# Performance work log

Measured on AMD Instinct MI355X. Metric: run time of the kernel, lower is better.

The kernel has to match this reference:

```python
import jax, jax.numpy as jnp
import numpy as np
from jax.scipy.special import logsumexp

B, T, F = 32, 256, 32   # batch, line width (time), line height (features)
HID = 128
VOCAB = 100             # blank index = VOCAB
LBL = 32                # label length
NEG = -1e30


def _mdlstm(x, Wx, Wh1, Wh2, b):
    # x: [B, H, W, C] -> 2D LSTM: outer scan over width, inner scan over height
    Bb, H, W, C = x.shape
    hid = Wh1.shape[0]

    def col_step(carry, x_col):
        c_left, h_left = carry  # [H, B, hid] states from previous column

        def row_step(rc, inp):
            c_up, h_up = rc          # [B, hid] from previous row
            x_ij, c_l, h_l = inp     # [B, C], [B, hid], [B, hid]
            z = x_ij @ Wx + h_l @ Wh1 + h_up @ Wh2 + b  # [B, 5*hid]
            i_, g_, f1, f2, o_ = jnp.split(z, 5, axis=-1)
            c = jax.nn.sigmoid(f1) * c_l + jax.nn.sigmoid(f2) * c_up + jax.nn.sigmoid(i_) * jnp.tanh(g_)
            h = jax.nn.sigmoid(o_) * jnp.tanh(c)
            return (c, h), (c, h)

        z0 = jnp.zeros((Bb, hid), x.dtype)
        _, (c_col, h_col) = jax.lax.scan(row_step, (z0, z0), (x_col, c_left, h_left))
        return (c_col, h_col), h_col

    x_t = jnp.transpose(x, (2, 1, 0, 3))  # [W, H, B, C]
    zc = jnp.zeros((H, Bb, hid), x.dtype)
    _, hs = jax.lax.scan(col_step, (zc, zc), x_t)  # [W, H, B, hid]
    return jnp.transpose(hs, (2, 1, 0, 3))  # [B, H, W, hid]


def _ctc_loss(logp, labels, blank):
    # logp: [B, T, V] log-softmax; labels: [B, L] int in [0, blank)
    Bb, Tt, V = logp.shape
    Ll = labels.shape[1]
    S = 2 * Ll + 1
    ext = jnp.full((Bb, S), blank, dtype=labels.dtype).at[:, 1::2].set(labels)  # blank-interleaved
    lp_ext = jnp.take_along_axis(logp, jnp.broadcast_to(ext[:, None, :], (Bb, Tt, S)), axis=2)  # [B,T,S]
    prev2 = jnp.concatenate([jnp.full((Bb, 2), blank, dtype=ext.dtype), ext[:, :-2]], axis=1)
    skip = (ext != blank) & (ext != prev2)
    skip = skip.at[:, :2].set(False)
    alpha0 = jnp.full((Bb, S), NEG, logp.dtype).at[:, 0].set(lp_ext[:, 0, 0]).at[:, 1].set(lp_ext[:, 0, 1])

    def step(alpha, lp_t):
        a1 = jnp.concatenate([jnp.full((Bb, 1), NEG, alpha.dtype), alpha[:, :-1]], axis=1)
        a2 = jnp.concatenate([jnp.full((Bb, 2), NEG, alpha.dtype), alpha[:, :-2]], axis=1)
        a2 = jnp.where(skip, a2, NEG)
        new = logsumexp(jnp.stack([alpha, a1, a2], axis=0), axis=0) + lp_t
        return new, None

    alphaT, _ = jax.lax.scan(step, alpha0, jnp.transpose(lp_ext, (1, 0, 2))[1:])
    ll = logsumexp(jnp.stack([alphaT[:, -1], alphaT[:, -2]], axis=0), axis=0)
    return -ll  # [B]


def setup_inputs() -> dict:
    key = jax.random.key(0)
    ks = jax.random.split(key, 8)
    s = 0.08
    return {
        "X": jax.random.normal(ks[0], (B, T, F), jnp.float32),
        "y": jax.random.randint(ks[1], (B, LBL), 0, VOCAB),
        "Wx": jax.random.normal(ks[2], (1, 5 * HID), jnp.float32) * s,
        "Wh1": jax.random.normal(ks[3], (HID, 5 * HID), jnp.float32) * s,
        "Wh2": jax.random.normal(ks[4], (HID, 5 * HID), jnp.float32) * s,
        "b": jax.random.normal(ks[5], (5 * HID,), jnp.float32) * 0.01,
        "W_fc": jax.random.normal(ks[6], (HID, VOCAB + 1), jnp.float32) * s,
        "b_fc": jax.random.normal(ks[7], (VOCAB + 1,), jnp.float32) * 0.01,
    }


def reference(X, y, Wx, Wh1, Wh2, b, W_fc, b_fc):
    x = jnp.transpose(X, (0, 2, 1))[..., None]        # [B, F, T, 1] (image)
    h = _mdlstm(x, Wx, Wh1, Wh2, b)                    # [B, F, T, HID]
    feat = jnp.sum(h, axis=1)                          # collapse over height -> [B, T, HID]
    logits = feat @ W_fc + b_fc                        # [B, T, VOCAB+1]
    logp = jax.nn.log_softmax(logits, axis=-1)
    return _ctc_loss(logp, y, VOCAB)                   # per-example CTC loss [B]
```

## Files before the change

kernel.cpp:

```cpp
#include <hip/hip_runtime.h>

#define NEGF (-1e30f)

typedef __attribute__((ext_vector_type(8))) short short8;
typedef __attribute__((ext_vector_type(4))) float float4v;

template <bool V> struct BC { static constexpr bool value = V; };

__device__ __forceinline__ short f2bf(float f) {
  union { float f; unsigned u; } v; v.f = f;
  unsigned r = v.u + 0x7fffu + ((v.u >> 16) & 1u);
  return (short)(r >> 16);
}
__device__ __forceinline__ float fastrcp(float x) { return __builtin_amdgcn_rcpf(x); }
__device__ __forceinline__ float sigf(float x) { return fastrcp(1.0f + __expf(-x)); }
__device__ __forceinline__ float tanhfast(float x) { return 1.0f - 2.0f * fastrcp(__expf(2.0f * x) + 1.0f); }

__global__ void prep_w_kernel(const float* __restrict__ Wh1, const float* __restrict__ Wh2,
                              short* __restrict__ wsW) {
  int t = blockIdx.x * 256 + threadIdx.x;
  int lane = t & 63;
  int frag = t >> 6;
  int nt = frag >> 3, kk = frag & 7;
  int n  = nt * 16 + (lane & 15);
  int kb = kk * 32 + (lane >> 4) * 8;
  short8 v;
#pragma unroll
  for (int j = 0; j < 8; ++j) {
    int k = kb + j;
    float w = (k < 128) ? Wh1[k * 640 + n] : Wh2[(k - 128) * 640 + n];
    v[j] = f2bf(w);
  }
  ((short8*)wsW)[frag * 64 + lane] = v;
}

__global__ __launch_bounds__(512)
void mdlstm_kernel(const float* __restrict__ X, const short* __restrict__ wsW,
                   const float* __restrict__ Wx, const float* __restrict__ bias,
                   float* __restrict__ feat) {
  __shared__ __align__(16) short h_buf[2][32][136];
  __shared__ __align__(16) short wlds[128 * 512];

  const int b    = blockIdx.x;
  const int tid  = threadIdx.x;
  const int lane = tid & 63;
  const int g    = tid >> 6;
  const int col  = lane & 15;
  const int quad = lane >> 4;
  const int jj   = g * 16 + col;

  for (int i = tid; i < 2 * 32 * 136 / 2; i += 512) ((int*)h_buf)[i] = 0;
  {
    const uint4* src = (const uint4*)(wsW + 192 * 512);
    uint4* dst = (uint4*)wlds;
    for (int i = tid; i < 8192; i += 512) dst[i] = src[i];
  }
  {
    float4 z4 = {0.f, 0.f, 0.f, 0.f};
    float4* f4 = (float4*)(feat + b * 32768);
    for (int i = tid; i < 8192; i += 512) f4[i] = z4;
  }

  float wx[5], bg[5];
#pragma unroll
  for (int q = 0; q < 5; ++q) {
    wx[q] = Wx[q * 128 + jj];
    bg[q] = bias[q * 128 + jj];
  }
  float cp[2][4];
#pragma unroll
  for (int mt = 0; mt < 2; ++mt)
#pragma unroll
    for (int r = 0; r < 4; ++r) cp[mt][r] = 0.0f;

  const float* Xg = X + b * 8192;
  float* fb = feat + b * 32768;
  const short8* W8 = (const short8*)wsW;
  const int col48 = col + 48;
  __syncthreads();

  auto step = [&](int d, auto c0, auto c1, auto cv) {
    constexpr bool DO0 = decltype(c0)::value;
    constexpr bool DO1 = decltype(c1)::value;
    constexpr bool ALLV = decltype(cv)::value;
    const int rbuf = (d + 1) & 1, wbuf = d & 1;

    float4v acc[5][2];
#pragma unroll
    for (int q = 0; q < 5; ++q) {
      if (DO0) acc[q][0] = (float4v){bg[q], bg[q], bg[q], bg[q]};
      if (DO1) acc[q][1] = (float4v){bg[q], bg[q], bg[q], bg[q]};
    }
    const short8 z8 = (short8){0, 0, 0, 0, 0, 0, 0, 0};
#pragma unroll
    for (int kk = 0; kk < 8; ++kk) {
      const int up = (kk >= 4) ? 1 : 0;
      const int cc = (kk & 3) * 32 + quad * 8;
      short8 a0, a1;
      if (DO0) {
        int row = col - up;
        a0 = (row >= 0) ? *(const short8*)&h_buf[rbuf][row][cc] : z8;
      }
      if (DO1) {
        int row = 16 + col - up;
        a1 = *(const short8*)&h_buf[rbuf][row][cc];
      }
#pragma unroll
      for (int q = 0; q < 5; ++q) {
        short8 bf;
        if (q < 3) bf = W8[((q * 8 + g) * 8 + kk) * 64 + lane];
        else       bf = *(const short8*)&wlds[(((q - 3) * 8 + g) * 8 + kk) * 512 + lane * 8];
        if (DO0) acc[q][0] = __builtin_amdgcn_mfma_f32_16x16x32_bf16(a0, bf, acc[q][0], 0, 0, 0);
        if (DO1) acc[q][1] = __builtin_amdgcn_mfma_f32_16x16x32_bf16(a1, bf, acc[q][1], 0, 0, 0);
      }
    }

    float t0 = __shfl_up(cp[0][3], 16);
    float t1 = __shfl_up(cp[1][3], 16);
    float tx = __shfl(cp[0][3], col48);
    float cuA[4] = {quad ? t0 : 0.0f, cp[0][0], cp[0][1], cp[0][2]};
    float cuB[4] = {quad ? t1 : tx,   cp[1][0], cp[1][1], cp[1][2]};

    float fo[2][4], xm[2][4];
#pragma unroll
    for (int mt = 0; mt < 2; ++mt) {
      if ((mt == 0 && !DO0) || (mt == 1 && !DO1)) continue;
      const int m0 = mt * 16 + quad * 4;
#pragma unroll
      for (int r = 0; r < 4; ++r) {
        int w = d - (m0 + r);
        if (ALLV || (w >= 0 && w < 256)) {
          fo[mt][r] = fb[w * 128 + jj];
          xm[mt][r] = Xg[w * 32 + (m0 + r)];
        }
      }
    }
#pragma unroll
    for (int mt = 0; mt < 2; ++mt) {
      if ((mt == 0 && !DO0) || (mt == 1 && !DO1)) continue;
      const int m0 = mt * 16 + quad * 4;
#pragma unroll
      for (int r = 0; r < 4; ++r) {
        const int m = m0 + r;
        const int w = d - m;
        if (ALLV || (w >= 0 && w < 256)) {
          float c_up = mt ? cuB[r] : cuA[r];
          float c_l  = cp[mt][r];
          float x    = xm[mt][r];
          float zi = fmaf(x, wx[0], acc[0][mt][r]);
          float zg = fmaf(x, wx[1], acc[1][mt][r]);
          float z1 = fmaf(x, wx[2], acc[2][mt][r]);
          float z2 = fmaf(x, wx[3], acc[3][mt][r]);
          float zo = fmaf(x, wx[4], acc[4][mt][r]);
          float c = sigf(z1) * c_l + sigf(z2) * c_up + sigf(zi) * tanhfast(zg);
          float h = sigf(zo) * tanhfast(c);
          cp[mt][r] = c;
          h_buf[wbuf][m][jj] = f2bf(h);
          fb[w * 128 + jj] = fo[mt][r] + h;
        }
      }
    }
  };

  BC<true> T; BC<false> F;
  for (int d = 0;   d < 16;  ++d) { step(d, T, F, F); __syncthreads(); }
  for (int d = 16;  d < 31;  ++d) { step(d, T, T, F); __syncthreads(); }
  for (int d = 31;  d < 256; ++d) { step(d, T, T, T); __syncthreads(); }
  for (int d = 256; d < 271; ++d) { step(d, T, T, F); __syncthreads(); }
  for (int d = 271; d < 287; ++d) { step(d, F, T, F); __syncthreads(); }
}

__global__ __launch_bounds__(256)
void logits_kernel(const float* __restrict__ feat, const float* __restrict__ Wfc,
                   const float* __restrict__ bfc, float* __restrict__ logp) {
  __shared__ float sW[128 * 101];
  __shared__ float sF[8][128];
  __shared__ float sL[8][104];
  __shared__ float sLse[8];
  const int tid = threadIdx.x;
  const int b  = blockIdx.x >> 5;
  const int t0 = (blockIdx.x & 31) * 8;

  for (int i = tid; i < 128 * 101; i += 256) sW[i] = Wfc[i];
  for (int i = tid; i < 8 * 128; i += 256)
    sF[i >> 7][i & 127] = feat[(b * 256 + t0 + (i >> 7)) * 128 + (i & 127)];
  __syncthreads();
  for (int idx = tid; idx < 8 * 101; idx += 256) {
    int tr = idx / 101, v = idx - tr * 101;
    float s = bfc[v];
#pragma unroll 4
    for (int k = 0; k < 128; ++k) s += sF[tr][k] * sW[k * 101 + v];
    sL[tr][v] = s;
  }
  __syncthreads();
  if (tid < 8) {
    float m = NEGF;
    for (int v = 0; v < 101; ++v) m = fmaxf(m, sL[tid][v]);
    float su = 0.0f;
    for (int v = 0; v < 101; ++v) su += __expf(sL[tid][v] - m);
    sLse[tid] = m + __logf(su);
  }
  __syncthreads();
  for (int idx = tid; idx < 8 * 101; idx += 256) {
    int tr = idx / 101, v = idx - tr * 101;
    logp[(b * 256 + t0 + tr) * 101 + v] = sL[tr][v] - sLse[tr];
  }
}

__global__ __launch_bounds__(64)
void ctc_kernel(const float* __restrict__ logp, const int* __restrict__ y,
                float* __restrict__ out) {
  const int b = blockIdx.x;
  const int l = threadIdx.x;
  const float* lpb = logp + b * 256 * 101;
  const int* yb = y + b * 32;
  int lab = (l & 1) ? yb[l >> 1] : 100;
  bool skip = (l & 1) && (l >= 3) && (yb[l >> 1] != yb[(l >> 1) - 1]);

  float a   = (l == 0) ? lpb[100] : ((l == 1) ? lpb[lab] : NEGF);
  float a64 = NEGF;
  float pl[4], pb[4];
#pragma unroll
  for (int tt = 0; tt < 4; ++tt) {
    pl[tt] = lpb[(1 + tt) * 101 + lab];
    pb[tt] = lpb[(1 + tt) * 101 + 100];
  }
#pragma unroll 4
  for (int t = 1; t < 256; ++t) {
    const int s = (t - 1) & 3;
    float lpl = pl[s], lpbk = pb[s];
    if (t + 4 < 256) {
      pl[s] = lpb[(t + 4) * 101 + lab];
      pb[s] = lpb[(t + 4) * 101 + 100];
    }
    float am1 = __shfl_up(a, 1); if (l == 0) am1 = NEGF;
    float am2 = __shfl_up(a, 2); if (l < 2 || !skip) am2 = NEGF;
    float m3 = fmaxf(a, fmaxf(am1, am2));
    float na = m3 + __logf(__expf(a - m3) + __expf(am1 - m3) + __expf(am2 - m3)) + lpl;
    float m2 = fmaxf(a64, a);
    float na64 = m2 + __logf(__expf(a64 - m2) + __expf(a - m2)) + lpbk;
    a = na;
    a64 = na64;
  }
  float A63 = __shfl(a, 63);
  float A64 = __shfl(a64, 63);
  if (l == 0) {
    float m = fmaxf(A63, A64);
    out[b] = -(m + __logf(__expf(A63 - m) + __expf(A64 - m)));
  }
}

extern "C" void kernel_launch(void* const* d_in, const int* in_sizes, int n_in,
                              void* d_out, int out_size, void* d_ws, size_t ws_size,
                              hipStream_t stream) {
  const float* X   = (const float*)d_in[0];
  const int*   y   = (const int*)d_in[1];
  const float* Wx  = (const float*)d_in[2];
  const float* Wh1 = (const float*)d_in[3];
  const float* Wh2 = (const float*)d_in[4];
  const float* bi  = (const float*)d_in[5];
  const float* Wfc = (const float*)d_in[6];
  const float* bfc = (const float*)d_in[7];
  float* out = (float*)d_out;

  char* ws = (char*)d_ws;
  short* wsW  = (short*)(ws);
  float* feat = (float*)(ws + 0x50000);
  float* logp = (float*)(ws + 0x450000);

  prep_w_kernel<<<80, 256, 0, stream>>>(Wh1, Wh2, wsW);
  mdlstm_kernel<<<32, 512, 0, stream>>>(X, wsW, Wx, bi, feat);
  logits_kernel<<<1024, 256, 0, stream>>>(feat, Wfc, bfc, logp);
  ctc_kernel<<<32, 64, 0, stream>>>(logp, y, out);
}
```

Baseline: 983.5 us.

## Prefetch first global weight fragments, cache a gate slice in LDS, enlarge logits tiles

In the MDLSTM recurrence, the kk=0 fragments for gates 0 and 1 are loaded from global memory during the previous step and kept in registers. The kk=0 fragment of gate 2 is moved into an extra LDS buffer. The MFMA order is changed so the LDS-resident gates issue first, which hides global load latency on the serial diagonal critical path. The logits kernel now handles 32 time rows per block instead of 8, with vectorised feature loads, so the W_fc copy into shared memory is repeated four times less often. The costs are more register pressure and more LDS use.

```diff
diff --git a/kernel.cpp b/kernel.cpp
--- a/kernel.cpp
+++ b/kernel.cpp
@@ -40,6 +40,7 @@
                    float* __restrict__ feat) {
   __shared__ __align__(16) short h_buf[2][32][136];
   __shared__ __align__(16) short wlds[128 * 512];
+  __shared__ __align__(16) short wlds2[8 * 512];
 
   const int b    = blockIdx.x;
   const int tid  = threadIdx.x;
@@ -54,6 +55,12 @@
     const uint4* src = (const uint4*)(wsW + 192 * 512);
     uint4* dst = (uint4*)wlds;
     for (int i = tid; i < 8192; i += 512) dst[i] = src[i];
+    const uint4* s2 = (const uint4*)wsW;
+    uint4* d2 = (uint4*)wlds2;
+    for (int i = tid; i < 512; i += 512) {
+      int gg = i >> 6, ln = i & 63;
+      d2[i] = s2[(128 + 8 * gg) * 64 + ln];
+    }
   }
   {
     float4 z4 = {0.f, 0.f, 0.f, 0.f};
@@ -77,6 +84,9 @@
   float* fb = feat + b * 32768;
   const short8* W8 = (const short8*)wsW;
   const int col48 = col + 48;
+
+  short8 pf0 = W8[((0 * 8 + g) * 8 + 0) * 64 + lane];
+  short8 pf1 = W8[((1 * 8 + g) * 8 + 0) * 64 + lane];
   __syncthreads();
 
   auto step = [&](int d, auto c0, auto c1, auto cv) {
@@ -105,13 +115,28 @@
         int row = 16 + col - up;
         a1 = *(const short8*)&h_buf[rbuf][row][cc];
       }
-#pragma unroll
-      for (int q = 0; q < 5; ++q) {
-        short8 bf;
-        if (q < 3) bf = W8[((q * 8 + g) * 8 + kk) * 64 + lane];
-        else       bf = *(const short8*)&wlds[(((q - 3) * 8 + g) * 8 + kk) * 512 + lane * 8];
-        if (DO0) acc[q][0] = __builtin_amdgcn_mfma_f32_16x16x32_bf16(a0, bf, acc[q][0], 0, 0, 0);
-        if (DO1) acc[q][1] = __builtin_amdgcn_mfma_f32_16x16x32_bf16(a1, bf, acc[q][1], 0, 0, 0);
+      {
+        short8 b3 = *(const short8*)&wlds[((0 * 8 + g) * 8 + kk) * 512 + lane * 8];
+        if (DO0) acc[3][0] = __builtin_amdgcn_mfma_f32_16x16x32_bf16(a0, b3, acc[3][0], 0, 0, 0);
+        if (DO1) acc[3][1] = __builtin_amdgcn_mfma_f32_16x16x32_bf16(a1, b3, acc[3][1], 0, 0, 0);
+        short8 b4 = *(const short8*)&wlds[((1 * 8 + g) * 8 + kk) * 512 + lane * 8];
+        if (DO0) acc[4][0] = __builtin_amdgcn_mfma_f32_16x16x32_bf16(a0, b4, acc[4][0], 0, 0, 0);
+        if (DO1) acc[4][1] = __builtin_amdgcn_mfma_f32_16x16x32_bf16(a1, b4, acc[4][1], 0, 0, 0);
+      }
+      {
+        short8 b2;
+        if (kk == 0) b2 = *(const short8*)&wlds2[g * 512 + lane * 8];
+        else         b2 = W8[((2 * 8 + g) * 8 + kk) * 64 + lane];
+        if (DO0) acc[2][0] = __builtin_amdgcn_mfma_f32_16x16x32_bf16(a0, b2, acc[2][0], 0, 0, 0);
+        if (DO1) acc[2][1] = __builtin_amdgcn_mfma_f32_16x16x32_bf16(a1, b2, acc[2][1], 0, 0, 0);
+      }
+      {
+        short8 b0 = (kk == 0) ? pf0 : W8[((0 * 8 + g) * 8 + kk) * 64 + lane];
+        if (DO0) acc[0][0] = __builtin_amdgcn_mfma_f32_16x16x32_bf16(a0, b0, acc[0][0], 0, 0, 0);
+        if (DO1) acc[0][1] = __builtin_amdgcn_mfma_f32_16x16x32_bf16(a1, b0, acc[0][1], 0, 0, 0);
+        short8 b1 = (kk == 0) ? pf1 : W8[((1 * 8 + g) * 8 + kk) * 64 + lane];
+        if (DO0) acc[1][0] = __builtin_amdgcn_mfma_f32_16x16x32_bf16(a0, b1, acc[1][0], 0, 0, 0);
+        if (DO1) acc[1][1] = __builtin_amdgcn_mfma_f32_16x16x32_bf16(a1, b1, acc[1][1], 0, 0, 0);
       }
     }
 
@@ -160,6 +185,8 @@
         }
       }
     }
+    pf0 = W8[((0 * 8 + g) * 8 + 0) * 64 + lane];
+    pf1 = W8[((1 * 8 + g) * 8 + 0) * 64 + lane];
   };
 
   BC<true> T; BC<false> F;
@@ -174,18 +201,21 @@
 void logits_kernel(const float* __restrict__ feat, const float* __restrict__ Wfc,
                    const float* __restrict__ bfc, float* __restrict__ logp) {
   __shared__ float sW[128 * 101];
-  __shared__ float sF[8][128];
-  __shared__ float sL[8][104];
-  __shared__ float sLse[8];
+  __shared__ float sF[32][128];
+  __shared__ float sL[32][104];
+  __shared__ float sLse[32];
   const int tid = threadIdx.x;
-  const int b  = blockIdx.x >> 5;
-  const int t0 = (blockIdx.x & 31) * 8;
+  const int b  = blockIdx.x >> 3;
+  const int t0 = (blockIdx.x & 7) * 32;
 
   for (int i = tid; i < 128 * 101; i += 256) sW[i] = Wfc[i];
-  for (int i = tid; i < 8 * 128; i += 256)
-    sF[i >> 7][i & 127] = feat[(b * 256 + t0 + (i >> 7)) * 128 + (i & 127)];
+  {
+    const float4* src = (const float4*)(feat + (b * 256 + t0) * 128);
+    float4* dst = (float4*)sF;
+    for (int i = tid; i < 1024; i += 256) dst[i] = src[i];
+  }
   __syncthreads();
-  for (int idx = tid; idx < 8 * 101; idx += 256) {
+  for (int idx = tid; idx < 32 * 101; idx += 256) {
     int tr = idx / 101, v = idx - tr * 101;
     float s = bfc[v];
 #pragma unroll 4
@@ -193,7 +223,7 @@
     sL[tr][v] = s;
   }
   __syncthreads();
-  if (tid < 8) {
+  if (tid < 32) {
     float m = NEGF;
     for (int v = 0; v < 101; ++v) m = fmaxf(m, sL[tid][v]);
     float su = 0.0f;
@@ -201,7 +231,7 @@
     sLse[tid] = m + __logf(su);
   }
   __syncthreads();
-  for (int idx = tid; idx < 8 * 101; idx += 256) {
+  for (int idx = tid; idx < 32 * 101; idx += 256) {
     int tr = idx / 101, v = idx - tr * 101;
     logp[(b * 256 + t0 + tr) * 101 + v] = sL[tr][v] - sLse[tr];
   }
@@ -270,6 +300,6 @@
 
   prep_w_kernel<<<80, 256, 0, stream>>>(Wh1, Wh2, wsW);
   mdlstm_kernel<<<32, 512, 0, stream>>>(X, wsW, Wx, bi, feat);
-  logits_kernel<<<1024, 256, 0, stream>>>(feat, Wfc, bfc, logp);
+  logits_kernel<<<256, 256, 0, stream>>>(feat, Wfc, bfc, logp);
   ctc_kernel<<<32, 64, 0, stream>>>(logp, y, out);
 }
```

After: 996.7 us. About the same (+1.3%).

## Accumulate height-summed features in an LDS ring buffer instead of global RMW

Applied to the files above, without the earlier changes.

Each recurrence step used to load and store the global feature accumulator for every active cell, a read-modify-write on the serial critical path. The accumulation now goes into a 33-slot shared-memory ring indexed by column. Each column is flushed to global once all 32 rows have contributed, which also removes the initial zero-fill of the feature buffer. To free LDS for the ring, the weight tile kept in shared memory shrinks slightly, so a few B-fragments for one wave are read from global memory instead.

```diff
diff --git a/kernel.cpp b/kernel.cpp
--- a/kernel.cpp
+++ b/kernel.cpp
@@ -39,7 +39,8 @@
                    const float* __restrict__ Wx, const float* __restrict__ bias,
                    float* __restrict__ feat) {
   __shared__ __align__(16) short h_buf[2][32][136];
-  __shared__ __align__(16) short wlds[128 * 512];
+  __shared__ __align__(16) short wlds[125 * 512];
+  __shared__ float ring[33 * 132];
 
   const int b    = blockIdx.x;
   const int tid  = threadIdx.x;
@@ -53,13 +54,9 @@
   {
     const uint4* src = (const uint4*)(wsW + 192 * 512);
     uint4* dst = (uint4*)wlds;
-    for (int i = tid; i < 8192; i += 512) dst[i] = src[i];
-  }
-  {
-    float4 z4 = {0.f, 0.f, 0.f, 0.f};
-    float4* f4 = (float4*)(feat + b * 32768);
-    for (int i = tid; i < 8192; i += 512) f4[i] = z4;
-  }
+    for (int i = tid; i < 8000; i += 512) dst[i] = src[i];
+  }
+  for (int i = tid; i < 33 * 132; i += 512) ring[i] = 0.0f;
 
   float wx[5], bg[5];
 #pragma unroll
@@ -78,12 +75,22 @@
   const short8* W8 = (const short8*)wsW;
   const int col48 = col + 48;
   __syncthreads();
+
+  auto flush = [&](int d) {
+    int wf = d - 32;
+    if (wf >= 0 && tid < 128) {
+      int sf = wf % 33;
+      fb[wf * 128 + tid] = ring[sf * 132 + tid];
+      ring[sf * 132 + tid] = 0.0f;
+    }
+  };
 
   auto step = [&](int d, auto c0, auto c1, auto cv) {
     constexpr bool DO0 = decltype(c0)::value;
     constexpr bool DO1 = decltype(c1)::value;
     constexpr bool ALLV = decltype(cv)::value;
     const int rbuf = (d + 1) & 1, wbuf = d & 1;
+    const int sd = d % 33;
 
     float4v acc[5][2];
 #pragma unroll
@@ -107,11 +114,13 @@
       }
 #pragma unroll
       for (int q = 0; q < 5; ++q) {
-        short8 bf;
-        if (q < 3) bf = W8[((q * 8 + g) * 8 + kk) * 64 + lane];
-        else       bf = *(const short8*)&wlds[(((q - 3) * 8 + g) * 8 + kk) * 512 + lane * 8];
-        if (DO0) acc[q][0] = __builtin_amdgcn_mfma_f32_16x16x32_bf16(a0, bf, acc[q][0], 0, 0, 0);
-        if (DO1) acc[q][1] = __builtin_amdgcn_mfma_f32_16x16x32_bf16(a1, bf, acc[q][1], 0, 0, 0);
+        short8 bw;
+        if (q < 3)       bw = W8[((q * 8 + g) * 8 + kk) * 64 + lane];
+        else if (q == 3) bw = *(const short8*)&wlds[((g * 8 + kk)) * 512 + lane * 8];
+        else if (g == 7 && kk >= 5) bw = W8[((4 * 8 + 7) * 8 + kk) * 64 + lane];
+        else             bw = *(const short8*)&wlds[((64 + g * 8 + kk)) * 512 + lane * 8];
+        if (DO0) acc[q][0] = __builtin_amdgcn_mfma_f32_16x16x32_bf16(a0, bw, acc[q][0], 0, 0, 0);
+        if (DO1) acc[q][1] = __builtin_amdgcn_mfma_f32_16x16x32_bf16(a1, bw, acc[q][1], 0, 0, 0);
       }
     }
 
@@ -121,7 +130,7 @@
     float cuA[4] = {quad ? t0 : 0.0f, cp[0][0], cp[0][1], cp[0][2]};
     float cuB[4] = {quad ? t1 : tx,   cp[1][0], cp[1][1], cp[1][2]};
 
-    float fo[2][4], xm[2][4];
+    float xm[2][4];
 #pragma unroll
     for (int mt = 0; mt < 2; ++mt) {
       if ((mt == 0 && !DO0) || (mt == 1 && !DO1)) continue;
@@ -129,10 +138,7 @@
 #pragma unroll
       for (int r = 0; r < 4; ++r) {
         int w = d - (m0 + r);
-        if (ALLV || (w >= 0 && w < 256)) {
-          fo[mt][r] = fb[w * 128 + jj];
-          xm[mt][r] = Xg[w * 32 + (m0 + r)];
-        }
+        if (ALLV || (w >= 0 && w < 256)) xm[mt][r] = Xg[w * 32 + (m0 + r)];
       }
     }
 #pragma unroll
@@ -156,18 +162,20 @@
           float h = sigf(zo) * tanhfast(c);
           cp[mt][r] = c;
           h_buf[wbuf][m][jj] = f2bf(h);
-          fb[w * 128 + jj] = fo[mt][r] + h;
+          int s = sd - m; s += (s >> 31) & 33;
+          ring[s * 132 + jj] += h;
         }
       }
     }
   };
 
   BC<true> T; BC<false> F;
-  for (int d = 0;   d < 16;  ++d) { step(d, T, F, F); __syncthreads(); }
-  for (int d = 16;  d < 31;  ++d) { step(d, T, T, F); __syncthreads(); }
-  for (int d = 31;  d < 256; ++d) { step(d, T, T, T); __syncthreads(); }
-  for (int d = 256; d < 271; ++d) { step(d, T, T, F); __syncthreads(); }
-  for (int d = 271; d < 287; ++d) { step(d, F, T, F); __syncthreads(); }
+  for (int d = 0;   d < 16;  ++d) { flush(d); step(d, T, F, F); __syncthreads(); }
+  for (int d = 16;  d < 31;  ++d) { flush(d); step(d, T, T, F); __syncthreads(); }
+  for (int d = 31;  d < 256; ++d) { flush(d); step(d, T, T, T); __syncthreads(); }
+  for (int d = 256; d < 271; ++d) { flush(d); step(d, T, T, F); __syncthreads(); }
+  for (int d = 271; d < 287; ++d) { flush(d); step(d, F, T, F); __syncthreads(); }
+  if (tid < 128) fb[255 * 128 + tid] = ring[(255 % 33) * 132 + tid];
 }
 
 __global__ __launch_bounds__(256)
```

Result: slower. 1.028 ms (+4.5%).

## Share one reciprocal across LSTM gates and stage more weights in LDS

Applied to the files above, without the earlier changes.

Rewrites the gate nonlinearities so the cell update needs a single reciprocal over a common denominator. Inputs are clamped to ±15 so the exponentials do not overflow. A slice of the third gate's weights is copied into a second LDS buffer, the MFMA weight loads are reordered to start with LDS operands, and addresses are computed from precomputed base pointers to reduce integer work. The risks are lower precision from the product-of-denominators form and a change in behaviour near saturation from the clamps.

```diff
diff --git a/kernel.cpp b/kernel.cpp
--- a/kernel.cpp
+++ b/kernel.cpp
@@ -13,8 +13,7 @@
   return (short)(r >> 16);
 }
 __device__ __forceinline__ float fastrcp(float x) { return __builtin_amdgcn_rcpf(x); }
-__device__ __forceinline__ float sigf(float x) { return fastrcp(1.0f + __expf(-x)); }
-__device__ __forceinline__ float tanhfast(float x) { return 1.0f - 2.0f * fastrcp(__expf(2.0f * x) + 1.0f); }
+__device__ __forceinline__ float clamp15(float x) { return fminf(15.0f, fmaxf(-15.0f, x)); }
 
 __global__ void prep_w_kernel(const float* __restrict__ Wh1, const float* __restrict__ Wh2,
                               short* __restrict__ wsW) {
@@ -40,6 +39,7 @@
                    float* __restrict__ feat) {
   __shared__ __align__(16) short h_buf[2][32][136];
   __shared__ __align__(16) short wlds[128 * 512];
+  __shared__ __align__(16) short wlds2[8 * 512];
 
   const int b    = blockIdx.x;
   const int tid  = threadIdx.x;
@@ -54,6 +54,12 @@
     const uint4* src = (const uint4*)(wsW + 192 * 512);
     uint4* dst = (uint4*)wlds;
     for (int i = tid; i < 8192; i += 512) dst[i] = src[i];
+    const uint4* s2 = (const uint4*)wsW;
+    uint4* d2 = (uint4*)wlds2;
+    for (int i = tid; i < 512; i += 512) {
+      int gg = i >> 6, ln = i & 63;
+      d2[i] = s2[(128 + 8 * gg) * 64 + ln];
+    }
   }
   {
     float4 z4 = {0.f, 0.f, 0.f, 0.f};
@@ -77,6 +83,16 @@
   float* fb = feat + b * 32768;
   const short8* W8 = (const short8*)wsW;
   const int col48 = col + 48;
+
+  const short8* pW0 = W8 + ((0 * 8 + g) * 8) * 64 + lane;
+  const short8* pW1 = W8 + ((1 * 8 + g) * 8) * 64 + lane;
+  const short8* pW2 = W8 + ((2 * 8 + g) * 8) * 64 + lane;
+  const short8* pL3 = (const short8*)&wlds[((0 * 8 + g) * 8) * 512 + lane * 8];
+  const short8* pL4 = (const short8*)&wlds[((1 * 8 + g) * 8) * 512 + lane * 8];
+  const short8* pL2 = (const short8*)&wlds2[g * 512 + lane * 8];
+  const float*  pX  = Xg - 31 * (quad * 4);
+  float*        pF0 = fb + jj - 128 * (quad * 4);
+  float*        pF1 = fb + jj - 128 * (16 + quad * 4);
   __syncthreads();
 
   auto step = [&](int d, auto c0, auto c1, auto cv) {
@@ -105,13 +121,26 @@
         int row = 16 + col - up;
         a1 = *(const short8*)&h_buf[rbuf][row][cc];
       }
-#pragma unroll
-      for (int q = 0; q < 5; ++q) {
-        short8 bf;
-        if (q < 3) bf = W8[((q * 8 + g) * 8 + kk) * 64 + lane];
-        else       bf = *(const short8*)&wlds[(((q - 3) * 8 + g) * 8 + kk) * 512 + lane * 8];
-        if (DO0) acc[q][0] = __builtin_amdgcn_mfma_f32_16x16x32_bf16(a0, bf, acc[q][0], 0, 0, 0);
-        if (DO1) acc[q][1] = __builtin_amdgcn_mfma_f32_16x16x32_bf16(a1, bf, acc[q][1], 0, 0, 0);
+      {
+        short8 b3 = pL3[kk * 64];
+        if (DO0) acc[3][0] = __builtin_amdgcn_mfma_f32_16x16x32_bf16(a0, b3, acc[3][0], 0, 0, 0);
+        if (DO1) acc[3][1] = __builtin_amdgcn_mfma_f32_16x16x32_bf16(a1, b3, acc[3][1], 0, 0, 0);
+        short8 b4 = pL4[kk * 64];
+        if (DO0) acc[4][0] = __builtin_amdgcn_mfma_f32_16x16x32_bf16(a0, b4, acc[4][0], 0, 0, 0);
+        if (DO1) acc[4][1] = __builtin_amdgcn_mfma_f32_16x16x32_bf16(a1, b4, acc[4][1], 0, 0, 0);
+      }
+      {
+        short8 b2 = (kk == 0) ? pL2[0] : pW2[kk * 64];
+        if (DO0) acc[2][0] = __builtin_amdgcn_mfma_f32_16x16x32_bf16(a0, b2, acc[2][0], 0, 0, 0);
+        if (DO1) acc[2][1] = __builtin_amdgcn_mfma_f32_16x16x32_bf16(a1, b2, acc[2][1], 0, 0, 0);
+      }
+      {
+        short8 b0 = pW0[kk * 64];
+        if (DO0) acc[0][0] = __builtin_amdgcn_mfma_f32_16x16x32_bf16(a0, b0, acc[0][0], 0, 0, 0);
+        if (DO1) acc[0][1] = __builtin_amdgcn_mfma_f32_16x16x32_bf16(a1, b0, acc[0][1], 0, 0, 0);
+        short8 b1 = pW1[kk * 64];
+        if (DO0) acc[1][0] = __builtin_amdgcn_mfma_f32_16x16x32_bf16(a0, b1, acc[1][0], 0, 0, 0);
+        if (DO1) acc[1][1] = __builtin_amdgcn_mfma_f32_16x16x32_bf16(a1, b1, acc[1][1], 0, 0, 0);
       }
     }
 
@@ -121,6 +150,8 @@
     float cuA[4] = {quad ? t0 : 0.0f, cp[0][0], cp[0][1], cp[0][2]};
     float cuB[4] = {quad ? t1 : tx,   cp[1][0], cp[1][1], cp[1][2]};
 
+    const float* pXd = pX + d * 32;
+    float* pFd[2] = {pF0 + d * 128, pF1 + d * 128};
     float fo[2][4], xm[2][4];
 #pragma unroll
     for (int mt = 0; mt < 2; ++mt) {
@@ -130,8 +161,8 @@
       for (int r = 0; r < 4; ++r) {
         int w = d - (m0 + r);
         if (ALLV || (w >= 0 && w < 256)) {
-          fo[mt][r] = fb[w * 128 + jj];
-          xm[mt][r] = Xg[w * 32 + (m0 + r)];
+          fo[mt][r] = pFd[mt][-128 * r];
+          xm[mt][r] = pXd[-31 * (mt * 16 + r)];
         }
       }
     }
@@ -147,16 +178,22 @@
           float c_up = mt ? cuB[r] : cuA[r];
           float c_l  = cp[mt][r];
           float x    = xm[mt][r];
-          float zi = fmaf(x, wx[0], acc[0][mt][r]);
-          float zg = fmaf(x, wx[1], acc[1][mt][r]);
-          float z1 = fmaf(x, wx[2], acc[2][mt][r]);
-          float z2 = fmaf(x, wx[3], acc[3][mt][r]);
-          float zo = fmaf(x, wx[4], acc[4][mt][r]);
-          float c = sigf(z1) * c_l + sigf(z2) * c_up + sigf(zi) * tanhfast(zg);
-          float h = sigf(zo) * tanhfast(c);
+          float zi = clamp15(fmaf(x, wx[0], acc[0][mt][r]));
+          float zg = clamp15(fmaf(x, wx[1], acc[1][mt][r]));
+          float z1 = clamp15(fmaf(x, wx[2], acc[2][mt][r]));
+          float z2 = clamp15(fmaf(x, wx[3], acc[3][mt][r]));
+          float zo = clamp15(fmaf(x, wx[4], acc[4][mt][r]));
+          float e1 = __expf(z1), e2 = __expf(z2), ei = __expf(zi), eg = __expf(2.0f * zg);
+          float A1 = 1.0f + e1, A2 = 1.0f + e2, Ai = 1.0f + ei, G = 1.0f + eg;
+          float P = Ai * G, Q = A1 * A2;
+          float rD = fastrcp(P * Q);
+          float c = (e1 * c_l * (A2 * P) + e2 * c_up * (A1 * P) + ei * (eg - 1.0f) * Q) * rD;
+          float eo = __expf(-zo);
+          float ec = __expf(2.0f * clamp15(c));
+          float h = (ec - 1.0f) * fastrcp((1.0f + eo) * (ec + 1.0f));
           cp[mt][r] = c;
           h_buf[wbuf][m][jj] = f2bf(h);
-          fb[w * 128 + jj] = fo[mt][r] + h;
+          pFd[mt][-128 * r] = fo[mt][r] + h;
         }
       }
     }
```

After: 960.9 us. 1.02x faster.
